# Optimization experiments

Hardware: AMD Instinct MI355X
Metric: run time of the kernel (lower is better)

Reference implementation:

```python
import jax, jax.numpy as jnp
import numpy as np

B, T, G, M, D = 8, 2048, 2, 1024, 256
ALPHA = -1.0      # config['dist_to_logits_alpha']
TAU = 2.0         # curr_temp = max_temp at init
EPS = 1e-10


def setup_inputs() -> dict:
    key = jax.random.key(0)
    k1, k2, k3 = jax.random.split(key, 3)
    x = jax.random.normal(k1, (B, T, G * D), dtype=jnp.float32)
    # nn.init.uniform_(embedding, -0.999, 0.999)
    embedding = jax.random.uniform(k2, (G, M, D), dtype=jnp.float32, minval=-0.999, maxval=0.999)
    # uniform noise for gumbel sampling, clipped away from {0,1}
    gumbel_u = jax.random.uniform(k3, (B * T, G, M), dtype=jnp.float32, minval=1e-6, maxval=1.0 - 1e-6)
    return {"x": x, "embedding": embedding, "gumbel_u": gumbel_u}


def reference(x, embedding, gumbel_u):
    b, t, c = x.shape
    g, m, d = embedding.shape
    xf = x.reshape(-1, g, d)                                  # [N, G, D]

    sq_e = jnp.sum(embedding ** 2, axis=-1)                   # [G, M]
    sq_x = jnp.sum(xf ** 2, axis=-1, keepdims=True)           # [N, G, 1]
    cross = jnp.einsum('ngd,gmd->ngm', xf, embedding)         # [N, G, M]
    logits = ALPHA * (sq_e[None] + sq_x - 2.0 * cross)        # [N, G, M]

    # hard-assignment code perplexity
    hard_x = jax.nn.one_hot(jnp.argmax(logits, axis=-1), m, dtype=logits.dtype)
    hard_probs = hard_x.mean(axis=0)                          # [G, M]
    code_perplexity = -jnp.sum(hard_probs * jnp.log2(hard_probs + EPS), axis=-1)

    # soft-assignment prob perplexity
    avg_probs = jax.nn.softmax(logits, axis=-1).mean(axis=0)  # [G, M]
    prob_perplexity = -jnp.sum(avg_probs * jnp.log2(avg_probs + EPS), axis=-1)

    # gumbel-softmax (hard=True, straight-through)
    gumbels = -jnp.log(-jnp.log(gumbel_u))
    y_soft = jax.nn.softmax((logits + gumbels) / TAU, axis=-1)
    idx = jnp.argmax(y_soft, axis=-1)                         # [N, G]
    y_hard = jax.nn.one_hot(idx, m, dtype=y_soft.dtype)
    st = y_hard + y_soft - jax.lax.stop_gradient(y_soft)      # straight-through one-hot

    # weighted sum over the codebook (avoids [N, G, M, D] blowup of the original)
    quantized = jnp.einsum('ngm,gmd->ngd', st, embedding).reshape(b, t, c)

    quantization_inds = idx.reshape(b, t, g).astype(jnp.int32)
    # use_vq_loss=True: F.mse_loss(x, quantized.detach())
    commitment_loss = jnp.mean((x - jax.lax.stop_gradient(quantized)) ** 2)

    return quantized, code_perplexity, prob_perplexity, quantization_inds, commitment_loss
```

## Files before the change

kernel.cpp:

```cpp
#include <hip/hip_runtime.h>
#include <math.h>

#define NTOT 16384
#define GG 2
#define MM 1024
#define DD 256

#define OFF_Q  ((size_t)0)
#define OFF_CP ((size_t)8388608)
#define OFF_PP ((size_t)8388610)
#define OFF_I  ((size_t)8388612)
#define OFF_L  ((size_t)8421380)

#define SHIFT 40.0f
#define REFINE_GAP 0.03f

typedef __attribute__((ext_vector_type(8))) short bf16x8;
typedef __attribute__((ext_vector_type(4))) float f32x4;
typedef unsigned short u16;
typedef unsigned int u32;

__device__ inline float wave_sum_f(float v) {
#pragma unroll
  for (int o = 32; o > 0; o >>= 1) v += __shfl_xor(v, o);
  return v;
}
__device__ inline u16 f2bf(float f) {
  u32 u = __float_as_uint(f);
  return (u16)((u + 0x7fffu + ((u >> 16) & 1u)) >> 16);
}
__device__ inline float bf2f(u16 h) {
  return __uint_as_float(((u32)h) << 16);
}
__device__ inline void async16(const void* g, void* l) {
  __builtin_amdgcn_global_load_lds(
      (const __attribute__((address_space(1))) u32*)g,
      (__attribute__((address_space(3))) u32*)l, 16, 0, 0);
}

#define WS_INVZ   32768
#define WS_EHSW   163840
#define WS_ELSW   1212416
#define WS_EST    2260992
#define WS_NEED3  (2260992ull + 2ull * MM * (size_t)NTOT * GG)

__global__ void vq_init2(const float* __restrict__ emb, float* __restrict__ sq_e,
                         float* __restrict__ avg, int* __restrict__ hist,
                         double* __restrict__ loss, u16* __restrict__ eh,
                         u16* __restrict__ el, int do_split) {
  const int row = blockIdx.x * 4 + (threadIdx.x >> 6);
  const int lane = threadIdx.x & 63;
  float4 e4 = *(const float4*)&emb[(size_t)row * DD + lane * 4];
  float s = e4.x * e4.x + e4.y * e4.y + e4.z * e4.z + e4.w * e4.w;
  s = wave_sum_f(s);
  if (do_split) {
    ushort4 h, l;
    h.x = f2bf(e4.x); l.x = f2bf(e4.x - bf2f(h.x));
    h.y = f2bf(e4.y); l.y = f2bf(e4.y - bf2f(h.y));
    h.z = f2bf(e4.z); l.z = f2bf(e4.z - bf2f(h.z));
    h.w = f2bf(e4.w); l.w = f2bf(e4.w - bf2f(h.w));
    *(ushort4*)&eh[(size_t)row * DD + lane * 4] = h;
    *(ushort4*)&el[(size_t)row * DD + lane * 4] = l;
  }
  if (lane == 0) sq_e[row] = s;
  if (blockIdx.x == 0) {
    for (int i = threadIdx.x; i < GG * MM; i += 256) { avg[i] = 0.f; hist[i] = 0; }
    if (threadIdx.x == 0) *loss = 0.0;
  }
}

__global__ void vq_init_swz(const float* __restrict__ emb, u16* __restrict__ eh_sw,
                            u16* __restrict__ el_sw) {
  int tid = blockIdx.x * 256 + threadIdx.x;
  int g = tid >> 15, rem = tid & 32767;
  int col = rem >> 5, kc = rem & 31;
  const float* src = emb + ((size_t)(g * MM + col)) * DD + kc * 8;
  float4 fa = *(const float4*)src;
  float4 fb = *(const float4*)(src + 4);
  float f[8] = {fa.x, fa.y, fa.z, fa.w, fb.x, fb.y, fb.z, fb.w};
  u16 hi[8], lo[8];
#pragma unroll
  for (int j = 0; j < 8; ++j) {
    hi[j] = f2bf(f[j]);
    lo[j] = f2bf(f[j] - bf2f(hi[j]));
  }
  int ct = col >> 6, cg = (col >> 4) & 3, l15 = col & 15;
  int ks = kc >> 2, quad = kc & 3;
  size_t chunk = ((((size_t)g * 16 + ct) * 8 + ks) * 4 + cg) * 64 + quad * 16 + l15;
  ushort4* dh = (ushort4*)(eh_sw + chunk * 8);
  ushort4* dl = (ushort4*)(el_sw + chunk * 8);
  dh[0] = make_ushort4(hi[0], hi[1], hi[2], hi[3]);
  dh[1] = make_ushort4(hi[4], hi[5], hi[6], hi[7]);
  dl[0] = make_ushort4(lo[0], lo[1], lo[2], lo[3]);
  dl[1] = make_ushort4(lo[4], lo[5], lo[6], lo[7]);
}

__global__ __launch_bounds__(512, 2) void vq_main3(
    const float* __restrict__ x, const float* __restrict__ emb,
    const float* __restrict__ gum, const float* __restrict__ sq_e,
    const u16* __restrict__ eh_sw, const u16* __restrict__ el_sw,
    float* __restrict__ out, u16* __restrict__ est, float* __restrict__ invZ_ws,
    int* __restrict__ hist, double* __restrict__ loss) {
  __shared__ u16 bt[2][32768];
  __shared__ int fidx_lds[128];

  const int g = blockIdx.y;
  const int n0 = blockIdx.x * 128;
  const int t = threadIdx.x;
  const int wave = t >> 6, lane = t & 63;
  const int quad = lane >> 4, l15 = lane & 15;
  const int nw = n0 + wave * 16;

  float* xs = (float*)&bt[0][0];
  {
    const float* xb = x + (size_t)nw * (GG * DD) + (size_t)g * DD;
#pragma unroll 4
    for (int j = 0; j < 16; ++j) {
      float4 v = *(const float4*)(xb + (size_t)j * (GG * DD) + lane * 4);
      *(float4*)&xs[wave * 4096 + j * 256 + ((lane ^ (j & 7)) << 2)] = v;
    }
  }

  bf16x8 ah[8], al[8];
#pragma unroll
  for (int ks = 0; ks < 8; ++ks) {
    int row = l15;
    int c0 = ks * 8 + quad * 2;
    const float* base = &xs[wave * 4096 + row * 256];
    float4 f0 = *(const float4*)&base[((c0 ^ (row & 7)) << 2)];
    float4 f1 = *(const float4*)&base[(((c0 + 1) ^ (row & 7)) << 2)];
    float f[8] = {f0.x, f0.y, f0.z, f0.w, f1.x, f1.y, f1.z, f1.w};
#pragma unroll
    for (int j = 0; j < 8; ++j) {
      u16 h = f2bf(f[j]);
      ah[ks][j] = (short)h;
      al[ks][j] = (short)f2bf(f[j] - bf2f(h));
    }
  }
  __syncthreads();

  const u16* sgh = eh_sw + (size_t)g * 16 * 16384;
  const u16* sgl = el_sw + (size_t)g * 16 * 16384;

  auto stage = [&](int ct, int buf) {
    const u16* sh = sgh + (size_t)ct * 16384;
    const u16* sl = sgl + (size_t)ct * 16384;
    u16* dh = &bt[buf][0];
    u16* dl = &bt[buf][16384];
#pragma unroll
    for (int j = 0; j < 4; ++j) {
      int slot = j * 8 + wave;
      async16(sh + slot * 512 + lane * 8, dh + slot * 512);
      async16(sl + slot * 512 + lane * 8, dl + slot * 512);
    }
  };

  float Zl[4], hv[4], z1[4], z2[4];
  int hid[4], i1[4], i2[4];
#pragma unroll
  for (int i = 0; i < 4; ++i) {
    Zl[i] = 0.f; hv[i] = -INFINITY; z1[i] = -INFINITY; z2[i] = -INFINITY;
    hid[i] = 0; i1[i] = 0; i2[i] = 0;
  }

  stage(0, 0);

#pragma unroll 1
  for (int ct = 0; ct < 16; ++ct) {
    __syncthreads();
    if (ct < 15) stage(ct + 1, (ct + 1) & 1);
    const u16* bh_p = &bt[ct & 1][0];
    const u16* bl_p = &bt[ct & 1][16384];
#pragma unroll 1
    for (int cg = 0; cg < 4; ++cg) {
      const int colG = ct * 64 + cg * 16 + l15;
      float sqv = sq_e[g * MM + colG];
      float gv[4];
#pragma unroll
      for (int r = 0; r < 4; ++r)
        gv[r] = gum[((size_t)(nw + quad * 4 + r) * GG + g) * MM + colG];

      f32x4 c0 = {0,0,0,0}, c1 = {0,0,0,0}, c2 = {0,0,0,0};
#pragma unroll
      for (int ks = 0; ks < 8; ++ks) {
        int off = ((ks * 4 + cg) * 64 + lane) * 8;
        bf16x8 bh = *(const bf16x8*)(bh_p + off);
        bf16x8 bl = *(const bf16x8*)(bl_p + off);
        c0 = __builtin_amdgcn_mfma_f32_16x16x32_bf16(ah[ks], bh, c0, 0, 0, 0);
        c1 = __builtin_amdgcn_mfma_f32_16x16x32_bf16(ah[ks], bl, c1, 0, 0, 0);
        c2 = __builtin_amdgcn_mfma_f32_16x16x32_bf16(al[ks], bh, c2, 0, 0, 0);
      }
      ushort4 pk;
      u16* pp = (u16*)&pk;
#pragma unroll
      for (int r = 0; r < 4; ++r) {
        float lp = 2.f * (c0[r] + c1[r] + c2[r]) - sqv + SHIFT;
        float ev = expf(fminf(lp, 80.f));
        Zl[r] += ev;
        pp[r] = f2bf(ev);
        if (lp > hv[r]) { hv[r] = lp; hid[r] = colG; }
        float zz = lp - logf(-logf(gv[r]));
        if (zz > z1[r]) {
          z2[r] = z1[r]; i2[r] = i1[r];
          z1[r] = zz; i1[r] = colG;
        } else if (zz > z2[r]) {
          z2[r] = zz; i2[r] = colG;
        }
      }
      *(ushort4*)&est[((size_t)(g * MM + colG) << 14) + nw + quad * 4] = pk;
    }
  }

#pragma unroll 1
  for (int r = 0; r < 4; ++r) {
    const int row = wave * 16 + quad * 4 + r;
    const int n = n0 + row;
    float Zr = Zl[r], hvr = hv[r];
    int hir = hid[r];
    float v1 = z1[r], v2 = z2[r];
    int j1 = i1[r], j2 = i2[r];
#pragma unroll
    for (int o = 1; o <= 8; o <<= 1) {
      Zr += __shfl_xor(Zr, o);
      float ohv = __shfl_xor(hvr, o); int ohi = __shfl_xor(hir, o);
      if (ohv > hvr || (ohv == hvr && ohi < hir)) { hvr = ohv; hir = ohi; }
      float w1 = __shfl_xor(v1, o), w2 = __shfl_xor(v2, o);
      int k1 = __shfl_xor(j1, o), k2 = __shfl_xor(j2, o);
      if (w1 > v1 || (w1 == v1 && k1 < j1)) {
        if (v1 > w2 || (v1 == w2 && j1 < k2)) { v2 = v1; j2 = j1; }
        else { v2 = w2; j2 = k2; }
        v1 = w1; j1 = k1;
      } else if (w1 > v2 || (w1 == v2 && k1 < j2)) { v2 = w1; j2 = k1; }
    }
    int fidx = j1;
    if (v1 - v2 < REFINE_GAP) {
      const float* xrow = x + (size_t)n * (GG * DD) + (size_t)g * DD;
      const float* eA = emb + ((size_t)g * MM + j1) * DD;
      const float* eB = emb + ((size_t)g * MM + j2) * DD;
      double dA = 0, sA = 0, dB = 0, sB = 0;
#pragma unroll
      for (int k = 0; k < 16; ++k) {
        int d = l15 * 16 + k;
        double xv = (double)xrow[d];
        double ea = (double)eA[d], eb = (double)eB[d];
        dA += xv * ea; sA += ea * ea;
        dB += xv * eb; sB += eb * eb;
      }
#pragma unroll
      for (int o = 1; o <= 8; o <<= 1) {
        dA += __shfl_xor(dA, o); sA += __shfl_xor(sA, o);
        dB += __shfl_xor(dB, o); sB += __shfl_xor(sB, o);
      }
      double uA = (double)gum[((size_t)n * GG + g) * MM + j1];
      double uB = (double)gum[((size_t)n * GG + g) * MM + j2];
      double zA = 2.0 * dA - sA - log(-log(uA));
      double zB = 2.0 * dB - sB - log(-log(uB));
      if (zB > zA || (zB == zA && j2 < j1)) fidx = j2;
    }
    if (l15 == 0) {
      out[OFF_I + (size_t)n * GG + g] = (float)fidx;
      atomicAdd(&hist[g * MM + hir], 1);
      invZ_ws[g * NTOT + n] = 1.f / Zr;
      fidx_lds[row] = fidx;
    }
  }
  __syncthreads();

  {
    float ls = 0.f;
#pragma unroll 4
    for (int j = 0; j < 16; ++j) {
      int idx = j * 512 + t;
      int row = idx >> 6, f4 = idx & 63;
      int n = n0 + row, fi = fidx_lds[row];
      float4 e4 = *(const float4*)&emb[((size_t)g * MM + fi) * DD + f4 * 4];
      float4 x4 = *(const float4*)&x[(size_t)n * (GG * DD) + (size_t)g * DD + f4 * 4];
      *(float4*)&out[OFF_Q + (size_t)n * (GG * DD) + (size_t)g * DD + f4 * 4] = e4;
      float dx = x4.x - e4.x, dy = x4.y - e4.y, dz = x4.z - e4.z, dw = x4.w - e4.w;
      ls += dx * dx + dy * dy + dz * dz + dw * dw;
    }
    ls = wave_sum_f(ls);
    if (lane == 0) atomicAdd(loss, (double)ls);
  }
}

__global__ void vq_avg(const u16* __restrict__ est, const float* __restrict__ invZ,
                       float* __restrict__ avg) {
  int wid = blockIdx.x * 4 + (threadIdx.x >> 6);
  int lane = threadIdx.x & 63;
  const u16* base = est + ((size_t)wid << 14);
  const float* zp = invZ + ((wid >> 10) << 14);
  float acc = 0.f;
#pragma unroll 4
  for (int it = 0; it < 64; ++it) {
    int n = it * 256 + lane * 4;
    ushort4 e4 = *(const ushort4*)(base + n);
    float4 z4 = *(const float4*)(zp + n);
    acc += bf2f(e4.x) * z4.x + bf2f(e4.y) * z4.y +
           bf2f(e4.z) * z4.z + bf2f(e4.w) * z4.w;
  }
  acc = wave_sum_f(acc);
  if (lane == 0) avg[wid] = acc;
}

__global__ void vq_fin(const float* __restrict__ avg, const int* __restrict__ hist,
                       const double* __restrict__ loss, float* __restrict__ out) {
  int g = blockIdx.x, t = threadIdx.x;
  float cp = 0.f, pp = 0.f;
  for (int m = t; m < MM; m += 256) {
    float hp = (float)hist[g * MM + m] * (1.f / 16384.f);
    cp += hp * log2f(hp + 1e-10f);
    float ap = avg[g * MM + m] * (1.f / 16384.f);
    pp += ap * log2f(ap + 1e-10f);
  }
  cp = wave_sum_f(cp);
  pp = wave_sum_f(pp);
  __shared__ float sc[4], sp[4];
  int wave = t >> 6, lane = t & 63;
  if (lane == 0) { sc[wave] = cp; sp[wave] = pp; }
  __syncthreads();
  if (t == 0) {
    out[OFF_CP + g] = -(sc[0] + sc[1] + sc[2] + sc[3]);
    out[OFF_PP + g] = -(sp[0] + sp[1] + sp[2] + sp[3]);
    if (g == 0) out[OFF_L] = (float)(*loss * (1.0 / 8388608.0));
  }
}

__global__ __launch_bounds__(256, 3) void vq_main_fast(
    const float* __restrict__ x, const float* __restrict__ emb,
    const float* __restrict__ gum, const float* __restrict__ sq_e,
    const u16* __restrict__ eh, const u16* __restrict__ el,
    float* __restrict__ out, float* __restrict__ avg,
    int* __restrict__ hist, double* __restrict__ loss) {
  __shared__ u16 est_lds[4][16][264];
  __shared__ float colsum[MM];
  __shared__ float red[16][4][8];
  __shared__ float fin_invZ[16];
  __shared__ int fin_idx[16];

  const int g = blockIdx.y;
  const int n0 = blockIdx.x * 16;
  const int t = threadIdx.x;
  const int wave = t >> 6, lane = t & 63;
  const int quad = lane >> 4, l15 = lane & 15;
  const int wm0 = wave * 256;

  for (int i = t; i < MM; i += 256) colsum[i] = 0.f;

  bf16x8 ah[8], al[8];
  {
    const float* xr = x + (size_t)(n0 + l15) * (GG * DD) + (size_t)g * DD + quad * 8;
#pragma unroll
    for (int ks = 0; ks < 8; ++ks) {
      float4 fa = *(const float4*)(xr + ks * 32);
      float4 fb = *(const float4*)(xr + ks * 32 + 4);
      float f[8] = {fa.x, fa.y, fa.z, fa.w, fb.x, fb.y, fb.z, fb.w};
#pragma unroll
      for (int j = 0; j < 8; ++j) {
        u16 h = f2bf(f[j]);
        ah[ks][j] = (short)h;
        al[ks][j] = (short)f2bf(f[j] - bf2f(h));
      }
    }
  }
  const u16* ehb = eh + ((size_t)g * MM + wm0 + l15) * DD + quad * 8;
  const u16* elb = el + ((size_t)g * MM + wm0 + l15) * DD + quad * 8;
  const float* sqb = sq_e + g * MM + wm0 + l15;

  float Z[4] = {0.f, 0.f, 0.f, 0.f};
  float hv[4] = {-INFINITY, -INFINITY, -INFINITY, -INFINITY};
  int hid[4] = {0, 0, 0, 0};
  float z1[4] = {-INFINITY, -INFINITY, -INFINITY, -INFINITY};
  float z2[4] = {-INFINITY, -INFINITY, -INFINITY, -INFINITY};
  int i1[4] = {0, 0, 0, 0}, i2[4] = {0, 0, 0, 0};

#pragma unroll 2
  for (int tt = 0; tt < 16; ++tt) {
    float sqv = sqb[tt * 16];
    float gv[4];
#pragma unroll
    for (int r = 0; r < 4; ++r)
      gv[r] = gum[((size_t)(n0 + quad * 4 + r) * GG + g) * MM + wm0 + tt * 16 + l15];
    f32x4 a0 = {0,0,0,0}, a1 = {0,0,0,0}, a2 = {0,0,0,0};
#pragma unroll
    for (int ks = 0; ks < 8; ++ks) {
      bf16x8 bh = *(const bf16x8*)(ehb + (size_t)tt * 16 * DD + ks * 32);
      bf16x8 bl = *(const bf16x8*)(elb + (size_t)tt * 16 * DD + ks * 32);
      a0 = __builtin_amdgcn_mfma_f32_16x16x32_bf16(ah[ks], bh, a0, 0, 0, 0);
      a1 = __builtin_amdgcn_mfma_f32_16x16x32_bf16(ah[ks], bl, a1, 0, 0, 0);
      a2 = __builtin_amdgcn_mfma_f32_16x16x32_bf16(al[ks], bh, a2, 0, 0, 0);
    }
    const int colL = tt * 16 + l15;
    const int colG = wm0 + colL;
#pragma unroll
    for (int r = 0; r < 4; ++r) {
      float lp = 2.f * (a0[r] + a1[r] + a2[r]) - sqv + SHIFT;
      float ev = expf(fminf(lp, 80.f));
      Z[r] += ev;
      est_lds[wave][quad * 4 + r][colL] = f2bf(ev);
      if (lp > hv[r]) { hv[r] = lp; hid[r] = colG; }
      float zz = lp - logf(-logf(gv[r]));
      if (zz > z1[r]) { z2[r] = z1[r]; i2[r] = i1[r]; z1[r] = zz; i1[r] = colG; }
      else if (zz > z2[r]) { z2[r] = zz; i2[r] = colG; }
    }
  }
#pragma unroll
  for (int r = 0; r < 4; ++r) {
    float Zr = Z[r], hvr = hv[r];
    int hir = hid[r];
    float v1 = z1[r], v2 = z2[r];
    int j1 = i1[r], j2 = i2[r];
#pragma unroll
    for (int o = 1; o <= 8; o <<= 1) {
      Zr += __shfl_xor(Zr, o);
      float ohv = __shfl_xor(hvr, o); int ohi = __shfl_xor(hir, o);
      if (ohv > hvr || (ohv == hvr && ohi < hir)) { hvr = ohv; hir = ohi; }
      float w1 = __shfl_xor(v1, o), w2 = __shfl_xor(v2, o);
      int k1 = __shfl_xor(j1, o), k2 = __shfl_xor(j2, o);
      if (w1 > v1 || (w1 == v1 && k1 < j1)) {
        if (v1 > w2 || (v1 == w2 && j1 < k2)) { v2 = v1; j2 = j1; }
        else { v2 = w2; j2 = k2; }
        v1 = w1; j1 = k1;
      } else if (w1 > v2 || (w1 == v2 && k1 < j2)) { v2 = w1; j2 = k1; }
    }
    if (l15 == 0) {
      float* rp = red[quad * 4 + r][wave];
      rp[0] = Zr; rp[1] = hvr; rp[2] = __int_as_float(hir);
      rp[3] = v1; rp[4] = __int_as_float(j1);
      rp[5] = v2; rp[6] = __int_as_float(j2);
    }
  }
  __syncthreads();
  if (t < 16) {
    const int row = t, n = n0 + row;
    float Zf = 0.f, hvf = -INFINITY; int hif = 0;
    float v1 = -INFINITY, v2 = -INFINITY; int j1 = 0, j2 = 0;
    for (int w = 0; w < 4; ++w) {
      const float* rp = red[row][w];
      Zf += rp[0];
      float ohv = rp[1]; int ohi = __float_as_int(rp[2]);
      if (ohv > hvf || (ohv == hvf && ohi < hif)) { hvf = ohv; hif = ohi; }
      float w1 = rp[3], w2 = rp[5];
      int k1 = __float_as_int(rp[4]), k2 = __float_as_int(rp[6]);
      if (w1 > v1 || (w1 == v1 && k1 < j1)) {
        if (v1 > w2 || (v1 == w2 && j1 < k2)) { v2 = v1; j2 = j1; }
        else { v2 = w2; j2 = k2; }
        v1 = w1; j1 = k1;
      } else if (w1 > v2 || (w1 == v2 && k1 < j2)) { v2 = w1; j2 = k1; }
    }
    int fidx = j1;
    if (v1 - v2 < REFINE_GAP) {
      const float* xrow = x + (size_t)n * (GG * DD) + (size_t)g * DD;
      const float* eA = emb + ((size_t)g * MM + j1) * DD;
      const float* eB = emb + ((size_t)g * MM + j2) * DD;
      double dA = 0, sA = 0, dB = 0, sB = 0;
      for (int d = 0; d < DD; ++d) {
        double xv = xrow[d], ea = eA[d], eb = eB[d];
        dA += xv * ea; sA += ea * ea;
        dB += xv * eb; sB += eb * eb;
      }
      double uA = gum[((size_t)n * GG + g) * MM + j1];
      double uB = gum[((size_t)n * GG + g) * MM + j2];
      double zA = 2.0 * dA - sA - log(-log(uA));
      double zB = 2.0 * dB - sB - log(-log(uB));
      if (zB > zA || (zB == zA && j2 < j1)) fidx = j2;
    }
    out[OFF_I + (size_t)n * GG + g] = (float)fidx;
    atomicAdd(&hist[g * MM + hif], 1);
    fin_invZ[row] = 1.f / Zf;
    fin_idx[row] = fidx;
  }
  __syncthreads();
  {
    const int row = t >> 4, c = (t & 15) * 16;
    const int n = n0 + row, fidx = fin_idx[row];
    const float* er = emb + ((size_t)g * MM + fidx) * DD + c;
    const float* xq = x + (size_t)n * (GG * DD) + (size_t)g * DD + c;
    float* op = out + OFF_Q + (size_t)n * (GG * DD) + (size_t)g * DD + c;
    float ls = 0.f;
#pragma unroll
    for (int j = 0; j < 4; ++j) {
      float4 e4 = *(const float4*)(er + j * 4);
      float4 x4 = *(const float4*)(xq + j * 4);
      *(float4*)(op + j * 4) = e4;
      float dx = x4.x - e4.x, dy = x4.y - e4.y, dz = x4.z - e4.z, dw = x4.w - e4.w;
      ls += dx * dx + dy * dy + dz * dz + dw * dw;
    }
    ls = wave_sum_f(ls);
    if (lane == 0) atomicAdd(loss, (double)ls);
  }
  float iZ[4];
#pragma unroll
  for (int r = 0; r < 4; ++r) iZ[r] = fin_invZ[quad * 4 + r];
#pragma unroll 1
  for (int tt = 0; tt < 16; ++tt) {
    float v = 0.f;
#pragma unroll
    for (int r = 0; r < 4; ++r)
      v += bf2f(est_lds[wave][quad * 4 + r][tt * 16 + l15]) * iZ[r];
    v += __shfl_xor(v, 16);
    v += __shfl_xor(v, 32);
    if (lane < 16) colsum[wm0 + tt * 16 + lane] += v;
  }
  __syncthreads();
  for (int i = t; i < MM; i += 256) atomicAdd(&avg[g * MM + i], colsum[i]);
}

extern "C" void kernel_launch(void* const* d_in, const int* in_sizes, int n_in,
                              void* d_out, int out_size, void* d_ws, size_t ws_size,
                              hipStream_t stream) {
  const float* x = (const float*)d_in[0];
  const float* emb = (const float*)d_in[1];
  const float* gum = (const float*)d_in[2];
  float* out = (float*)d_out;

  float* sq_e = (float*)d_ws;
  float* avg = (float*)((char*)d_ws + 8192);
  int* hist = (int*)((char*)d_ws + 16384);
  double* loss = (double*)((char*)d_ws + 24576);

  if (ws_size >= WS_NEED3) {
    float* invZ = (float*)((char*)d_ws + WS_INVZ);
    u16* eh_sw = (u16*)((char*)d_ws + WS_EHSW);
    u16* el_sw = (u16*)((char*)d_ws + WS_ELSW);
    u16* est = (u16*)((char*)d_ws + WS_EST);
    vq_init2<<<512, 256, 0, stream>>>(emb, sq_e, avg, hist, loss, eh_sw, el_sw, 0);
    vq_init_swz<<<256, 256, 0, stream>>>(emb, eh_sw, el_sw);
    vq_main3<<<dim3(NTOT / 128, GG), 512, 0, stream>>>(
        x, emb, gum, sq_e, eh_sw, el_sw, out, est, invZ, hist, loss);
    vq_avg<<<512, 256, 0, stream>>>(est, invZ, avg);
    vq_fin<<<GG, 256, 0, stream>>>(avg, hist, loss, out);
  } else {
    u16* eh = (u16*)((char*)d_ws + 32768);
    u16* el = eh + (size_t)GG * MM * DD;
    vq_init2<<<512, 256, 0, stream>>>(emb, sq_e, avg, hist, loss, eh, el, 1);
    vq_main_fast<<<dim3(NTOT / 16, GG), 256, 0, stream>>>(
        x, emb, gum, sq_e, eh, el, out, avg, hist, loss);
    vq_fin<<<GG, 256, 0, stream>>>(avg, hist, loss, out);
  }
}
```

Before: 364.3 us.

## Use fast exp/log intrinsics in main loop and widen vq_avg reduction

Swaps expf/logf for __expf/__logf in the hot per-logit loop, with a series-based -log(u) for u near 1 to keep gumbel noise accurate. Rewrites vq_avg to use one block per codebook row, 16-byte loads and more blocks for better memory parallelism. Also fully unrolls the commitment-loss loop. The cheaper transcendentals cut ALU cost in the main kernel but add approximation error, which could change argmax ties near the refine gap.

```diff
diff --git a/kernel.cpp b/kernel.cpp
--- a/kernel.cpp
+++ b/kernel.cpp
@@ -36,6 +36,12 @@
   __builtin_amdgcn_global_load_lds(
       (const __attribute__((address_space(1))) u32*)g,
       (__attribute__((address_space(3))) u32*)l, 16, 0, 0);
+}
+__device__ inline float neg_log_acc(float u) {
+  float t1 = 1.0f - u;
+  float se = t1 * (1.f + t1 * (0.5f + t1 * (0.33333334f + t1 * 0.25f)));
+  float fl = -__logf(u);
+  return (t1 < 0.015625f) ? se : fl;
 }
 
 #define WS_INVZ   32768
@@ -195,11 +201,11 @@
 #pragma unroll
       for (int r = 0; r < 4; ++r) {
         float lp = 2.f * (c0[r] + c1[r] + c2[r]) - sqv + SHIFT;
-        float ev = expf(fminf(lp, 80.f));
+        float ev = __expf(fminf(lp, 80.f));
         Zl[r] += ev;
         pp[r] = f2bf(ev);
         if (lp > hv[r]) { hv[r] = lp; hid[r] = colG; }
-        float zz = lp - logf(-logf(gv[r]));
+        float zz = lp - __logf(neg_log_acc(gv[r]));
         if (zz > z1[r]) {
           z2[r] = z1[r]; i2[r] = i1[r];
           z1[r] = zz; i1[r] = colG;
@@ -268,7 +274,7 @@
 
   {
     float ls = 0.f;
-#pragma unroll 4
+#pragma unroll
     for (int j = 0; j < 16; ++j) {
       int idx = j * 512 + t;
       int row = idx >> 6, f4 = idx & 63;
@@ -286,21 +292,27 @@
 
 __global__ void vq_avg(const u16* __restrict__ est, const float* __restrict__ invZ,
                        float* __restrict__ avg) {
-  int wid = blockIdx.x * 4 + (threadIdx.x >> 6);
-  int lane = threadIdx.x & 63;
+  int wid = blockIdx.x;
+  int t = threadIdx.x;
   const u16* base = est + ((size_t)wid << 14);
   const float* zp = invZ + ((wid >> 10) << 14);
   float acc = 0.f;
-#pragma unroll 4
-  for (int it = 0; it < 64; ++it) {
-    int n = it * 256 + lane * 4;
-    ushort4 e4 = *(const ushort4*)(base + n);
-    float4 z4 = *(const float4*)(zp + n);
-    acc += bf2f(e4.x) * z4.x + bf2f(e4.y) * z4.y +
-           bf2f(e4.z) * z4.z + bf2f(e4.w) * z4.w;
+#pragma unroll
+  for (int it = 0; it < 8; ++it) {
+    int n = it * 2048 + t * 8;
+    uint4 e = *(const uint4*)(base + n);
+    float4 z0 = *(const float4*)(zp + n);
+    float4 z1 = *(const float4*)(zp + n + 4);
+    acc += bf2f((u16)(e.x & 0xffff)) * z0.x + bf2f((u16)(e.x >> 16)) * z0.y +
+           bf2f((u16)(e.y & 0xffff)) * z0.z + bf2f((u16)(e.y >> 16)) * z0.w +
+           bf2f((u16)(e.z & 0xffff)) * z1.x + bf2f((u16)(e.z >> 16)) * z1.y +
+           bf2f((u16)(e.w & 0xffff)) * z1.z + bf2f((u16)(e.w >> 16)) * z1.w;
   }
   acc = wave_sum_f(acc);
-  if (lane == 0) avg[wid] = acc;
+  __shared__ float sw[4];
+  if ((t & 63) == 0) sw[t >> 6] = acc;
+  __syncthreads();
+  if (t == 0) avg[wid] = sw[0] + sw[1] + sw[2] + sw[3];
 }
 
 __global__ void vq_fin(const float* __restrict__ avg, const int* __restrict__ hist,
@@ -528,7 +540,7 @@
     vq_init_swz<<<256, 256, 0, stream>>>(emb, eh_sw, el_sw);
     vq_main3<<<dim3(NTOT / 128, GG), 512, 0, stream>>>(
         x, emb, gum, sq_e, eh_sw, el_sw, out, est, invZ, hist, loss);
-    vq_avg<<<512, 256, 0, stream>>>(est, invZ, avg);
+    vq_avg<<<2048, 256, 0, stream>>>(est, invZ, avg);
     vq_fin<<<GG, 256, 0, stream>>>(avg, hist, loss, out);
   } else {
     u16* eh = (u16*)((char*)d_ws + 32768);
```

Result: no change. 359.4 us (-1.3%).
